# Kernel optimization log

Hardware: AMD Instinct MI355X
Metric: run time of the kernel (lower is better)

## Reference

```python
import jax, jax.numpy as jnp
import numpy as np
from jax import lax

N, E, G = 20000, 640000, 16
NA, H, NG, L, NC = 21, 128, 50, 6, 97
CUTOFF = 10.0
LOG2 = 0.6931471805599453

def ssp(v):
    # ShiftedSoftplus: softplus(x) - log(2)
    return jax.nn.softplus(v) - LOG2

def setup_inputs() -> dict:
    key = jax.random.key(0)
    ks = jax.random.split(key, 24)
    s = 0.08  # xavier-ish scale for 128-wide layers
    inp = {
        "x": jax.random.normal(ks[0], (N, NA), dtype=jnp.float32),
        "pos": jax.random.uniform(ks[1], (N, 3), dtype=jnp.float32, minval=0.0, maxval=30.0),
        "edge_index": jax.random.randint(ks[2], (2, E), 0, N, dtype=jnp.int64),
        "batch": jnp.sort(jax.random.randint(ks[3], (N,), 0, G, dtype=jnp.int64)),
        # embedding Linear(21 -> 128), weights stored [in, out]
        "emb_w": jax.random.normal(ks[4], (NA, H), dtype=jnp.float32) * 0.15,
        "emb_b": jnp.zeros((H,), dtype=jnp.float32),
        # per-interaction-block params, stacked over L layers
        "mlp1_w": jax.random.normal(ks[5], (L, NG, H), dtype=jnp.float32) * 0.12,
        "mlp1_b": jnp.zeros((L, H), dtype=jnp.float32),
        "mlp2_w": jax.random.normal(ks[6], (L, H, H), dtype=jnp.float32) * s,
        "mlp2_b": jnp.zeros((L, H), dtype=jnp.float32),
        "conv1_w": jax.random.normal(ks[7], (L, H, H), dtype=jnp.float32) * s,  # no bias
        "conv2_w": jax.random.normal(ks[8], (L, H, H), dtype=jnp.float32) * s,
        "conv2_b": jnp.zeros((L, H), dtype=jnp.float32),
        "lin_w": jax.random.normal(ks[9], (L, H, H), dtype=jnp.float32) * s,
        "lin_b": jnp.zeros((L, H), dtype=jnp.float32),
        # head (note: original reuses self.lin1 twice, act is ReLU, dropout eval=identity)
        "lin1_w": jax.random.normal(ks[10], (H, H), dtype=jnp.float32) * s,
        "lin1_b": jnp.zeros((H,), dtype=jnp.float32),
        "lin2_w": jax.random.normal(ks[11], (H, NC), dtype=jnp.float32) * s,
        "lin2_b": jnp.zeros((NC,), dtype=jnp.float32),
    }
    return inp

def reference(x, pos, edge_index, batch, emb_w, emb_b, mlp1_w, mlp1_b, mlp2_w,
              mlp2_b, conv1_w, conv2_w, conv2_b, lin_w, lin_b, lin1_w, lin1_b,
              lin2_w, lin2_b):
    row, col = edge_index[0], edge_index[1]  # source j, target i
    d = pos[row] - pos[col]                  # [E,3]
    edge_weight = jnp.sqrt(jnp.sum(d * d, axis=-1))  # [E]
    # Gaussian smearing
    offset = jnp.linspace(0.0, CUTOFF, NG)
    coeff = -0.5 / (offset[1] - offset[0]) ** 2
    edge_attr = jnp.exp(coeff * (edge_weight[:, None] - offset[None, :]) ** 2)  # [E,NG]
    # cosine cutoff
    C = 0.5 * (jnp.cos(edge_weight * jnp.pi / CUTOFF) + 1.0)  # [E]

    h = x @ emb_w + emb_b  # [N,H]

    def block(h, p):
        m1w, m1b, m2w, m2b, c1w, c2w, c2b, lw, lb = p
        # edge MLP filter times cutoff envelope
        Wf = (ssp(edge_attr @ m1w + m1b) @ m2w + m2b) * C[:, None]  # [E,H]
        hx = h @ c1w                                 # lin1 (no bias)
        msg = hx[row] * Wf                           # gather + modulate
        agg = jax.ops.segment_sum(msg, col, num_segments=N)  # scatter-add
        y = ssp(agg @ c2w + c2b)
        y = y @ lw + lb
        return h + y, None

    h, _ = lax.scan(block, h, (mlp1_w, mlp1_b, mlp2_w, mlp2_b,
                               conv1_w, conv2_w, conv2_b, lin_w, lin_b))

    h = jax.nn.relu(h @ lin1_w + lin1_b)
    # global mean pool
    ones = jnp.ones((N,), dtype=h.dtype)
    counts = jnp.maximum(jax.ops.segment_sum(ones, batch, num_segments=G), 1.0)
    graph_emb = jax.ops.segment_sum(h, batch, num_segments=G) / counts[:, None]  # [G,H]
    h2 = jax.nn.relu(graph_emb @ lin1_w + lin1_b)  # lin1 reused; dropout=identity (eval)
    out = h2 @ lin2_w + lin2_b                     # [G,NC]
    return graph_emb, out
```

## Files before the change

kernel.cpp:

```cpp
#include <hip/hip_runtime.h>
#include <hip/hip_bf16.h>

#define HD 128
#define NGAUSS 50
#define NLAYER 6
#define NGRAPH 16
#define NCLS 97
#define NTAB2 8192
#define WMAX 12.0f

typedef __attribute__((ext_vector_type(8))) short bf16x8;
typedef __attribute__((ext_vector_type(4))) float f32x4;
typedef __attribute__((ext_vector_type(8))) ushort u16x8;
typedef __attribute__((ext_vector_type(4))) ushort u16x4;

__device__ __forceinline__ float ssp_f(float x) {
    float e = __expf(-fabsf(x));
    return fmaxf(x, 0.0f) + __logf(0.5f + 0.5f * e);
}
__device__ __forceinline__ ushort f2bf(float f) {
    uint u = __float_as_uint(f);
    return (ushort)((u + 0x7FFFu + ((u >> 16) & 1u)) >> 16);
}
__device__ __forceinline__ float bf2f(ushort s) {
    return __uint_as_float(((uint)s) << 16);
}

__global__ void hist_kernel(const int* __restrict__ col, int* __restrict__ deg, int E) {
    int e = blockIdx.x * blockDim.x + threadIdx.x;
    if (e < E) atomicAdd(&deg[col[e]], 1);
}

__global__ void scan1_kernel(const int* __restrict__ deg, int* __restrict__ rowp,
                             int* __restrict__ bsum, int N) {
    __shared__ int sm[256];
    const int t = threadIdx.x, i = blockIdx.x * 256 + t;
    int v = (i < N) ? deg[i] : 0;
    sm[t] = v;
    __syncthreads();
    for (int off = 1; off < 256; off <<= 1) {
        int x = sm[t];
        int a = (t >= off) ? sm[t - off] : 0;
        __syncthreads();
        sm[t] = x + a;
        __syncthreads();
    }
    if (i < N) rowp[i] = sm[t] - v;
    if (t == 255) bsum[blockIdx.x] = sm[255];
}
__global__ void scan2_kernel(const int* __restrict__ bsum, int* __restrict__ boff,
                             int NB, int* __restrict__ rowpN) {
    __shared__ int sm[256];
    const int t = threadIdx.x;
    int v = (t < NB) ? bsum[t] : 0;
    sm[t] = v;
    __syncthreads();
    for (int off = 1; off < 256; off <<= 1) {
        int x = sm[t];
        int a = (t >= off) ? sm[t - off] : 0;
        __syncthreads();
        sm[t] = x + a;
        __syncthreads();
    }
    if (t < NB) boff[t] = sm[t] - v;
    if (t == 255) *rowpN = sm[255];
}
__global__ void scan3_kernel(int* __restrict__ rowp, const int* __restrict__ boff,
                             int* __restrict__ cursor, int N) {
    int i = blockIdx.x * blockDim.x + threadIdx.x;
    if (i < N) {
        int r = rowp[i] + boff[i >> 8];
        rowp[i] = r;
        cursor[i] = r;
    }
}

__global__ void fill_kernel(const int* __restrict__ row, const int* __restrict__ col,
                            const float* __restrict__ pos, int* __restrict__ cursor,
                            uint2* __restrict__ meta, int E) {
    int e = blockIdx.x * blockDim.x + threadIdx.x;
    if (e >= E) return;
    int c = col[e], r = row[e];
    int slot = atomicAdd(&cursor[c], 1);
    float dx = pos[r*3+0] - pos[c*3+0];
    float dy = pos[r*3+1] - pos[c*3+1];
    float dz = pos[r*3+2] - pos[c*3+2];
    float w = sqrtf(dx*dx + dy*dy + dz*dz);
    float cenv = 0.5f * (cosf(w * 0.31415926535897931f) + 1.0f);
    const float invDW = (float)(NTAB2 - 1) / WMAX;
    int i = (int)(w * invDW + 0.5f);
    i = min(i, NTAB2 - 1);
    uint w0 = ((uint)r) | (((uint)i) << 16);
    meta[slot] = make_uint2(w0, __float_as_uint(cenv));
}

__global__ void prep_kernel(const float* __restrict__ m1w, const float* __restrict__ c1w,
                            const float* __restrict__ c2w, const float* __restrict__ lw,
                            const float* __restrict__ l1w, const float* __restrict__ m2w,
                            ushort* __restrict__ m1T, ushort* __restrict__ nodeThi,
                            ushort* __restrict__ nodeTlo, ushort* __restrict__ m2T) {
    int idx = blockIdx.x * blockDim.x + threadIdx.x;
    const int S1 = 6*128*64, S2 = 19*128*128, S3 = 6*128*128;
    if (idx < S1) {
        int l = idx / 8192, r = idx % 8192, c = r / 64, k = r % 64;
        float v = (k < NGAUSS) ? m1w[(size_t)l*NGAUSS*128 + k*128 + c] : 0.0f;
        m1T[(size_t)l*8192 + c*64 + k] = f2bf(v);
    } else if (idx < S1 + S2) {
        int j = idx - S1;
        int m = j / 16384, r = j % 16384, c = r / 128, k = r % 128;
        const float* src;
        if (m < 6)       src = c1w + (size_t)m*16384;
        else if (m < 12) src = c2w + (size_t)(m-6)*16384;
        else if (m < 18) src = lw  + (size_t)(m-12)*16384;
        else             src = l1w;
        float v = src[k*128 + c];
        ushort hi = f2bf(v);
        nodeThi[(size_t)m*16384 + c*128 + k] = hi;
        nodeTlo[(size_t)m*16384 + c*128 + k] = f2bf(v - bf2f(hi));
    } else if (idx < S1 + S2 + S3) {
        int j = idx - S1 - S2;
        int l = j / 16384, r = j % 16384, c = r / 128, k = r % 128;
        m2T[(size_t)l*16384 + c*128 + k] = f2bf(m2w[(size_t)l*16384 + k*128 + c]);
    }
}

__global__ void embed_kernel(const float* __restrict__ x,
                             const float* __restrict__ emb_w, const float* __restrict__ emb_b,
                             float* __restrict__ h, int N) {
    int idx = blockIdx.x * blockDim.x + threadIdx.x;
    if (idx >= N * HD) return;
    int n = idx >> 7, t = idx & 127;
    float acc = emb_b[t];
    #pragma unroll
    for (int a = 0; a < 21; ++a) acc += x[n*21 + a] * emb_w[a*HD + t];
    h[idx] = acc;
}

__global__ __launch_bounds__(256, 2) void buildtab_kernel(
        const ushort* __restrict__ m1T_all, const ushort* __restrict__ m2T_all,
        const float* __restrict__ m1b_all, const float* __restrict__ m2b_all,
        ushort* __restrict__ Tb6) {
    __shared__ ushort A1[128 * 64];
    __shared__ ushort B1[128 * 64];
    __shared__ ushort U [128 * 128];
    char* A1b = (char*)A1;
    char* B1b = (char*)B1;
    char* Ub  = (char*)U;
    const int tid  = threadIdx.x;
    const int lane = tid & 63;
    const int wave = tid >> 6;
    const int l15  = lane & 15;
    const int kgrp = (lane >> 4) * 8;
    const int rbase = wave * 32;
    const int NTILES = NTAB2 / 128;
    const int layer = blockIdx.x / NTILES;
    const int mt    = blockIdx.x % NTILES;
    const ushort* m1T = m1T_all + (size_t)layer * 8192;
    const ushort* m2T = m2T_all + (size_t)layer * 16384;
    const float*  m1b = m1b_all + layer * HD;
    const float*  m2b = m2b_all + layer * HD;

    #pragma unroll
    for (int p = 0; p < 4; ++p) {
        int rr = p * 32 + (tid >> 3);
        int k8 = (tid & 7) * 8;
        u16x8 v = *reinterpret_cast<const u16x8*>(&m1T[(size_t)rr * 64 + k8]);
        *reinterpret_cast<u16x8*>(&B1b[rr*128 + ((2*k8) ^ ((rr & 7) << 4))]) = v;
    }

    float b1c[8], b2c[8];
    #pragma unroll
    for (int cb = 0; cb < 8; ++cb) { b1c[cb] = m1b[cb*16 + l15]; b2c[cb] = m2b[cb*16 + l15]; }

    const float step = 10.0f / 49.0f;
    const float coeff = -0.5f / (step * step);
    const float DW = WMAX / (float)(NTAB2 - 1);

    #pragma unroll
    for (int p = 0; p < 4; ++p) {
        int rr = p * 32 + (tid >> 3);
        int k8 = (tid & 7) * 8;
        float w = (float)(mt*128 + rr) * DW;
        u16x8 v;
        #pragma unroll
        for (int j = 0; j < 8; ++j) {
            int k = k8 + j;
            float d = w - (float)k * step;
            float g = (k < NGAUSS) ? __expf(coeff * d * d) : 0.0f;
            v[j] = f2bf(g);
        }
        *reinterpret_cast<u16x8*>(&A1b[rr*128 + ((2*k8) ^ ((rr & 7) << 4))]) = v;
    }
    __syncthreads();

    f32x4 acc1[2][8];
    #pragma unroll
    for (int i = 0; i < 2; ++i)
        #pragma unroll
        for (int j = 0; j < 8; ++j) { acc1[i][j].x=0.f; acc1[i][j].y=0.f; acc1[i][j].z=0.f; acc1[i][j].w=0.f; }
    #pragma unroll
    for (int ks = 0; ks < 2; ++ks) {
        int k = ks*32 + kgrp;
        bf16x8 af[2];
        #pragma unroll
        for (int rt = 0; rt < 2; ++rt) {
            int r = rbase + rt*16 + l15;
            af[rt] = *reinterpret_cast<const bf16x8*>(&A1b[r*128 + ((2*k) ^ ((r & 7) << 4))]);
        }
        #pragma unroll
        for (int cb = 0; cb < 8; ++cb) {
            int c = cb*16 + l15;
            bf16x8 bv = *reinterpret_cast<const bf16x8*>(&B1b[c*128 + ((2*k) ^ ((c & 7) << 4))]);
            acc1[0][cb] = __builtin_amdgcn_mfma_f32_16x16x32_bf16(af[0], bv, acc1[0][cb], 0, 0, 0);
            acc1[1][cb] = __builtin_amdgcn_mfma_f32_16x16x32_bf16(af[1], bv, acc1[1][cb], 0, 0, 0);
        }
    }
    #pragma unroll
    for (int rt = 0; rt < 2; ++rt) {
        #pragma unroll
        for (int cb = 0; cb < 8; ++cb) {
            int c = cb*16 + l15;
            #pragma unroll
            for (int i = 0; i < 4; ++i) {
                int rrow = rbase + rt*16 + (lane >> 4)*4 + i;
                ushort us = f2bf(ssp_f(acc1[rt][cb][i] + b1c[cb]));
                *reinterpret_cast<ushort*>(&Ub[rrow*256 + ((2*c) ^ ((rrow & 7) << 4))]) = us;
            }
        }
    }
    __syncthreads();

    f32x4 acc2[2][8];
    #pragma unroll
    for (int i = 0; i < 2; ++i)
        #pragma unroll
        for (int j = 0; j < 8; ++j) { acc2[i][j].x=0.f; acc2[i][j].y=0.f; acc2[i][j].z=0.f; acc2[i][j].w=0.f; }
    #pragma unroll
    for (int kh = 0; kh < 2; ++kh) {
        if (kh) __syncthreads();
        #pragma unroll
        for (int p = 0; p < 4; ++p) {
            int rr = p * 32 + (tid >> 3);
            int kk = (tid & 7) * 8;
            u16x8 v = *reinterpret_cast<const u16x8*>(&m2T[(size_t)rr*128 + kh*64 + kk]);
            *reinterpret_cast<u16x8*>(&A1b[rr*128 + ((2*kk) ^ ((rr & 7) << 4))]) = v;
        }
        __syncthreads();
        #pragma unroll
        for (int ks2 = 0; ks2 < 2; ++ks2) {
            int ku = kh*64 + ks2*32 + kgrp;
            int kb = ks2*32 + kgrp;
            bf16x8 af[2];
            #pragma unroll
            for (int rt = 0; rt < 2; ++rt) {
                int r = rbase + rt*16 + l15;
                af[rt] = *reinterpret_cast<const bf16x8*>(&Ub[r*256 + ((2*ku) ^ ((r & 7) << 4))]);
            }
            #pragma unroll
            for (int cb = 0; cb < 8; ++cb) {
                int c = cb*16 + l15;
                bf16x8 bv = *reinterpret_cast<const bf16x8*>(&A1b[c*128 + ((2*kb) ^ ((c & 7) << 4))]);
                acc2[0][cb] = __builtin_amdgcn_mfma_f32_16x16x32_bf16(af[0], bv, acc2[0][cb], 0, 0, 0);
                acc2[1][cb] = __builtin_amdgcn_mfma_f32_16x16x32_bf16(af[1], bv, acc2[1][cb], 0, 0, 0);
            }
        }
    }

    #pragma unroll
    for (int rt = 0; rt < 2; ++rt) {
        #pragma unroll
        for (int cb = 0; cb < 8; ++cb) {
            int c = cb*16 + l15;
            #pragma unroll
            for (int i = 0; i < 4; ++i) {
                int rrow = rbase + rt*16 + (lane >> 4)*4 + i;
                Tb6[((size_t)layer*NTAB2 + mt*128 + rrow) * HD + c] = f2bf(acc2[rt][cb][i] + b2c[cb]);
            }
        }
    }
}

template<int EPI>
__global__ __launch_bounds__(256) void gemv64_kernel(
        const float* __restrict__ A, const ushort* __restrict__ BThi,
        const ushort* __restrict__ BTlo, const float* __restrict__ bias,
        float* __restrict__ fdst, ushort* __restrict__ bdst, int mtiles) {
    __shared__ ushort Bw[128 * 256];
    __shared__ ushort A_[64 * 128];
    char* Bwb = (char*)Bw;
    char* Ab  = (char*)A_;
    const int tid  = threadIdx.x;
    const int lane = tid & 63;
    const int wave = tid >> 6;
    const int l15  = lane & 15;
    const int kgrp = (lane >> 4) * 8;
    const int rbase = wave * 16;

    #pragma unroll
    for (int p = 0; p < 16; ++p) {
        int idx = p * 256 + tid;
        int c = idx >> 5;
        int k8 = (idx & 31) * 8;
        const ushort* src = (k8 < 128) ? BThi : BTlo;
        u16x8 v = *reinterpret_cast<const u16x8*>(&src[(size_t)c*128 + (k8 & 127)]);
        *reinterpret_cast<u16x8*>(&Bwb[c*512 + ((2*k8) ^ ((c & 7) << 4))]) = v;
    }
    float bt[8];
    if (EPI == 4) {
        #pragma unroll
        for (int cb = 0; cb < 8; ++cb) bt[cb] = bias[cb*16 + l15];
    }
    __syncthreads();

    for (int mt = blockIdx.x; mt < mtiles; mt += gridDim.x) {
        #pragma unroll
        for (int p = 0; p < 8; ++p) {
            int rr = p * 8 + (tid >> 5);
            int k4 = (tid & 31) * 4;
            f32x4 v = *reinterpret_cast<const f32x4*>(&A[(size_t)(mt*64 + rr)*HD + k4]);
            u16x4 b;
            b.x = f2bf(v.x); b.y = f2bf(v.y); b.z = f2bf(v.z); b.w = f2bf(v.w);
            *reinterpret_cast<u16x4*>(&Ab[rr*256 + ((2*k4) ^ ((rr & 7) << 4))]) = b;
        }
        __syncthreads();

        bf16x8 af[4];
        {
            int r = rbase + l15;
            #pragma unroll
            for (int q = 0; q < 4; ++q)
                af[q] = *reinterpret_cast<const bf16x8*>(&Ab[r*256 + ((2*(q*32 + kgrp)) ^ ((r & 7) << 4))]);
        }
        f32x4 acc[8];
        #pragma unroll
        for (int j = 0; j < 8; ++j) { acc[j].x=0.f; acc[j].y=0.f; acc[j].z=0.f; acc[j].w=0.f; }
        #pragma unroll
        for (int ks = 0; ks < 8; ++ks) {
            int kB = ks*32 + kgrp;
            #pragma unroll
            for (int cb = 0; cb < 8; ++cb) {
                int c = cb*16 + l15;
                bf16x8 bv = *reinterpret_cast<const bf16x8*>(&Bwb[c*512 + ((2*kB) ^ ((c & 7) << 4))]);
                acc[cb] = __builtin_amdgcn_mfma_f32_16x16x32_bf16(af[ks & 3], bv, acc[cb], 0, 0, 0);
            }
        }

        #pragma unroll
        for (int cb = 0; cb < 8; ++cb) {
            int c = cb*16 + l15;
            #pragma unroll
            for (int i = 0; i < 4; ++i) {
                int row = mt*64 + rbase + (lane >> 4)*4 + i;
                size_t off = (size_t)row * HD + c;
                if (EPI == 4) fdst[off] = fmaxf(acc[cb][i] + bt[cb], 0.0f);
                else          bdst[off] = f2bf(acc[cb][i]);
            }
        }
        __syncthreads();
    }
}

__global__ __launch_bounds__(512, 1) void nodefused_kernel(
        const ushort* __restrict__ aggb,
        const ushort* __restrict__ c2hi, const ushort* __restrict__ c2lo,
        const float* __restrict__ c2b,
        const ushort* __restrict__ lwhi, const ushort* __restrict__ lwlo,
        const float* __restrict__ lb,
        float* __restrict__ h, int mtiles) {
    __shared__ ushort W1[128 * 256];
    __shared__ ushort W2[128 * 256];
    __shared__ ushort BUF[32 * 128];
    char* W1b = (char*)W1;
    char* W2b = (char*)W2;
    char* Bu  = (char*)BUF;
    const int tid  = threadIdx.x;
    const int lane = tid & 63;
    const int wave = tid >> 6;
    const int l15  = lane & 15;
    const int kgrp = (lane >> 4) * 8;
    const int wr = (wave & 1) * 16;
    const int wc = (wave >> 1) * 2;

    #pragma unroll
    for (int p = 0; p < 8; ++p) {
        int idx = p * 512 + tid;
        int c = idx >> 5;
        int k8 = (idx & 31) * 8;
        const ushort* s1 = (k8 < 128) ? c2hi : c2lo;
        u16x8 v1 = *reinterpret_cast<const u16x8*>(&s1[(size_t)c*128 + (k8 & 127)]);
        *reinterpret_cast<u16x8*>(&W1b[c*512 + ((2*k8) ^ ((c & 7) << 4))]) = v1;
        const ushort* s2 = (k8 < 128) ? lwhi : lwlo;
        u16x8 v2 = *reinterpret_cast<const u16x8*>(&s2[(size_t)c*128 + (k8 & 127)]);
        *reinterpret_cast<u16x8*>(&W2b[c*512 + ((2*k8) ^ ((c & 7) << 4))]) = v2;
    }
    float b1c[2], b2c[2];
    #pragma unroll
    for (int cb = 0; cb < 2; ++cb) {
        int c = (wc + cb)*16 + l15;
        b1c[cb] = c2b[c];
        b2c[cb] = lb[c];
    }
    __syncthreads();

    for (int mt = blockIdx.x; mt < mtiles; mt += gridDim.x) {
        {
            int rr = tid >> 4;
            int k8 = (tid & 15) * 8;
            u16x8 v = *reinterpret_cast<const u16x8*>(&aggb[(size_t)(mt*32 + rr)*HD + k8]);
            *reinterpret_cast<u16x8*>(&Bu[rr*256 + ((2*k8) ^ ((rr & 7) << 4))]) = v;
        }
        float hp[2][4];
        #pragma unroll
        for (int cb = 0; cb < 2; ++cb) {
            int c = (wc + cb)*16 + l15;
            #pragma unroll
            for (int i = 0; i < 4; ++i) {
                int row = mt*32 + wr + (lane >> 4)*4 + i;
                hp[cb][i] = h[(size_t)row * HD + c];
            }
        }
        __syncthreads();

        bf16x8 af[4];
        {
            int r = wr + l15;
            #pragma unroll
            for (int q = 0; q < 4; ++q)
                af[q] = *reinterpret_cast<const bf16x8*>(&Bu[r*256 + ((2*(q*32 + kgrp)) ^ ((r & 7) << 4))]);
        }
        f32x4 acc[2];
        #pragma unroll
        for (int j = 0; j < 2; ++j) { acc[j].x=0.f; acc[j].y=0.f; acc[j].z=0.f; acc[j].w=0.f; }
        #pragma unroll
        for (int ks = 0; ks < 8; ++ks) {
            int kB = ks*32 + kgrp;
            #pragma unroll
            for (int cb = 0; cb < 2; ++cb) {
                int c = (wc + cb)*16 + l15;
                bf16x8 bv = *reinterpret_cast<const bf16x8*>(&W1b[c*512 + ((2*kB) ^ ((c & 7) << 4))]);
                acc[cb] = __builtin_amdgcn_mfma_f32_16x16x32_bf16(af[ks & 3], bv, acc[cb], 0, 0, 0);
            }
        }
        __syncthreads();

        #pragma unroll
        for (int cb = 0; cb < 2; ++cb) {
            int c = (wc + cb)*16 + l15;
            #pragma unroll
            for (int i = 0; i < 4; ++i) {
                int rrow = wr + (lane >> 4)*4 + i;
                ushort us = f2bf(ssp_f(acc[cb][i] + b1c[cb]));
                *reinterpret_cast<ushort*>(&Bu[rrow*256 + ((2*c) ^ ((rrow & 7) << 4))]) = us;
            }
        }
        __syncthreads();

        {
            int r = wr + l15;
            #pragma unroll
            for (int q = 0; q < 4; ++q)
                af[q] = *reinterpret_cast<const bf16x8*>(&Bu[r*256 + ((2*(q*32 + kgrp)) ^ ((r & 7) << 4))]);
        }
        #pragma unroll
        for (int j = 0; j < 2; ++j) { acc[j].x=0.f; acc[j].y=0.f; acc[j].z=0.f; acc[j].w=0.f; }
        #pragma unroll
        for (int ks = 0; ks < 8; ++ks) {
            int kB = ks*32 + kgrp;
            #pragma unroll
            for (int cb = 0; cb < 2; ++cb) {
                int c = (wc + cb)*16 + l15;
                bf16x8 bv = *reinterpret_cast<const bf16x8*>(&W2b[c*512 + ((2*kB) ^ ((c & 7) << 4))]);
                acc[cb] = __builtin_amdgcn_mfma_f32_16x16x32_bf16(af[ks & 3], bv, acc[cb], 0, 0, 0);
            }
        }
        #pragma unroll
        for (int cb = 0; cb < 2; ++cb) {
            int c = (wc + cb)*16 + l15;
            #pragma unroll
            for (int i = 0; i < 4; ++i) {
                int row = mt*32 + wr + (lane >> 4)*4 + i;
                h[(size_t)row * HD + c] = hp[cb][i] + acc[cb][i] + b2c[cb];
            }
        }
        __syncthreads();
    }
}

__global__ __launch_bounds__(256) void gathersum_kernel(
        const ushort* __restrict__ Tb, const uint2* __restrict__ meta,
        const int* __restrict__ rowp, const ushort* __restrict__ hxb,
        ushort* __restrict__ aggb, int N) {
    const int lane = threadIdx.x & 63;
    const int n = blockIdx.x * 4 + (threadIdx.x >> 6);
    if (n >= N) return;
    const int c0 = lane * 2;
    const int s0 = rowp[n], s1 = rowp[n + 1];
    float al[4] = {0.f, 0.f, 0.f, 0.f};
    float ah[4] = {0.f, 0.f, 0.f, 0.f};
    int s = s0;
    for (; s + 8 <= s1; s += 8) {
        uint2 m[8];
        uint tv[8], hv[8];
        #pragma unroll
        for (int k = 0; k < 8; ++k) m[k] = meta[s + k];
        #pragma unroll
        for (int k = 0; k < 8; ++k) {
            tv[k] = *reinterpret_cast<const uint*>(&Tb[(size_t)(m[k].x >> 16) * HD + c0]);
            hv[k] = *reinterpret_cast<const uint*>(&hxb[(size_t)(m[k].x & 0xFFFFu) * HD + c0]);
        }
        #pragma unroll
        for (int k = 0; k < 8; ++k) {
            float cv = __uint_as_float(m[k].y);
            float glo = __uint_as_float(tv[k] << 16) * cv;
            float ghi = __uint_as_float(tv[k] & 0xFFFF0000u) * cv;
            al[k & 3] += glo * __uint_as_float(hv[k] << 16);
            ah[k & 3] += ghi * __uint_as_float(hv[k] & 0xFFFF0000u);
        }
    }
    for (; s < s1; ++s) {
        uint2 m0 = meta[s];
        uint tv = *reinterpret_cast<const uint*>(&Tb[(size_t)(m0.x >> 16) * HD + c0]);
        uint hv = *reinterpret_cast<const uint*>(&hxb[(size_t)(m0.x & 0xFFFFu) * HD + c0]);
        float cv = __uint_as_float(m0.y);
        al[0] += __uint_as_float(tv << 16) * cv * __uint_as_float(hv << 16);
        ah[0] += __uint_as_float(tv & 0xFFFF0000u) * cv * __uint_as_float(hv & 0xFFFF0000u);
    }
    float lo = (al[0] + al[1]) + (al[2] + al[3]);
    float hi = (ah[0] + ah[1]) + (ah[2] + ah[3]);
    uint out = ((uint)f2bf(lo)) | (((uint)f2bf(hi)) << 16);
    *reinterpret_cast<uint*>(&aggb[(size_t)n * HD + c0]) = out;
}

__global__ void pool_kernel(const float* __restrict__ h1, const int* __restrict__ batch,
                            float* __restrict__ gsum, float* __restrict__ gcnt, int N) {
    __shared__ float pool[NGRAPH][HD];
    __shared__ float cnt[NGRAPH];
    const int t = threadIdx.x;
    #pragma unroll
    for (int g = 0; g < NGRAPH; ++g) pool[g][t] = 0.0f;
    if (t < NGRAPH) cnt[t] = 0.0f;
    __syncthreads();
    int chunk = (N + gridDim.x - 1) / gridDim.x;
    int n0 = blockIdx.x * chunk, n1 = min(N, n0 + chunk);
    for (int n = n0; n < n1; ++n) {
        int b = batch[n];
        pool[b][t] += h1[(size_t)n * HD + t];
        if (t == 0) cnt[b] += 1.0f;
    }
    __syncthreads();
    #pragma unroll
    for (int g = 0; g < NGRAPH; ++g) atomicAdd(&gsum[g*HD + t], pool[g][t]);
    if (t < NGRAPH) atomicAdd(&gcnt[t], cnt[t]);
}

__global__ void finalize_kernel(const float* __restrict__ gsum, const float* __restrict__ gcnt,
                                const float* __restrict__ l1w, const float* __restrict__ l1b,
                                const float* __restrict__ l2w, const float* __restrict__ l2b,
                                float* __restrict__ d_out) {
    __shared__ float ge[HD];
    __shared__ float h2[HD];
    const int g = blockIdx.x, t = threadIdx.x;
    float cnt = fmaxf(gcnt[g], 1.0f);
    float v = gsum[g*HD + t] / cnt;
    d_out[g*HD + t] = v;
    ge[t] = v;
    __syncthreads();
    float acc = l1b[t];
    #pragma unroll 8
    for (int k = 0; k < HD; ++k) acc += ge[k] * l1w[k*HD + t];
    h2[t] = fmaxf(acc, 0.0f);
    __syncthreads();
    if (t < NCLS) {
        float o = l2b[t];
        #pragma unroll 8
        for (int k = 0; k < HD; ++k) o += h2[k] * l2w[k*NCLS + t];
        d_out[NGRAPH*HD + g*NCLS + t] = o;
    }
}

extern "C" void kernel_launch(void* const* d_in, const int* in_sizes, int n_in,
                              void* d_out, int out_size, void* d_ws, size_t ws_size,
                              hipStream_t stream) {
    const float* x     = (const float*)d_in[0];
    const float* pos   = (const float*)d_in[1];
    const int*   eidx  = (const int*)d_in[2];
    const int*   batch = (const int*)d_in[3];
    const float* emb_w = (const float*)d_in[4];
    const float* emb_b = (const float*)d_in[5];
    const float* m1w   = (const float*)d_in[6];
    const float* m1b   = (const float*)d_in[7];
    const float* m2w   = (const float*)d_in[8];
    const float* m2b   = (const float*)d_in[9];
    const float* c1w   = (const float*)d_in[10];
    const float* c2w   = (const float*)d_in[11];
    const float* c2b   = (const float*)d_in[12];
    const float* lw    = (const float*)d_in[13];
    const float* lb    = (const float*)d_in[14];
    const float* l1w   = (const float*)d_in[15];
    const float* l1b   = (const float*)d_in[16];
    const float* l2w   = (const float*)d_in[17];
    const float* l2b   = (const float*)d_in[18];

    const int N = in_sizes[0] / 21;
    const int E = in_sizes[2] / 2;
    const int* row = eidx;
    const int* col = eidx + E;
    const int NT64 = (N + 63) / 64;
    const int NT32 = (N + 31) / 32;
    const int NB   = (N + 255) / 256;
    const int Npad = NT64 * 64 + 64;

    size_t off = 0;
    char* base = (char*)d_ws;
    auto alloc = [&](size_t bytes) -> void* {
        off = (off + 255) & ~(size_t)255;
        void* p = base + off;
        off += bytes;
        return p;
    };
    int*    deg     = (int*)alloc((size_t)N * 4);
    int*    cursor  = (int*)alloc((size_t)N * 4);
    int*    rowp    = (int*)alloc((size_t)(N + 1) * 4);
    int*    bsum    = (int*)alloc(512 * 4);
    int*    boff    = (int*)alloc(512 * 4);
    uint2*  meta    = (uint2*)alloc((size_t)E * 8);
    float*  h       = (float*)alloc((size_t)Npad * HD * 4);
    ushort* hxb     = (ushort*)alloc((size_t)Npad * HD * 2);
    ushort* aggb    = (ushort*)alloc((size_t)Npad * HD * 2);
    float*  h1      = (float*)alloc((size_t)Npad * HD * 4);
    ushort* Tb6     = (ushort*)alloc((size_t)6 * NTAB2 * HD * 2);
    ushort* m1T     = (ushort*)alloc((size_t)6 * 128 * 64 * 2);
    ushort* nodeThi = (ushort*)alloc((size_t)19 * 128 * 128 * 2);
    ushort* nodeTlo = (ushort*)alloc((size_t)19 * 128 * 128 * 2);
    ushort* m2T     = (ushort*)alloc((size_t)6 * 128 * 128 * 2);
    float*  gsum    = (float*)alloc((size_t)NGRAPH * HD * 4);
    float*  gcnt    = (float*)alloc((size_t)NGRAPH * 4);

    prep_kernel<<<1792, 256, 0, stream>>>(m1w, c1w, c2w, lw, l1w, m2w,
                                          m1T, nodeThi, nodeTlo, m2T);
    hipMemsetAsync(deg, 0, (size_t)N * 4, stream);
    hist_kernel<<<(E + 255)/256, 256, 0, stream>>>(col, deg, E);
    scan1_kernel<<<NB, 256, 0, stream>>>(deg, rowp, bsum, N);
    scan2_kernel<<<1, 256, 0, stream>>>(bsum, boff, NB, rowp + N);
    scan3_kernel<<<NB, 256, 0, stream>>>(rowp, boff, cursor, N);
    fill_kernel<<<(E + 255)/256, 256, 0, stream>>>(row, col, pos, cursor, meta, E);
    buildtab_kernel<<<6 * (NTAB2/128), 256, 0, stream>>>(m1T, m2T, m1b, m2b, Tb6);
    embed_kernel<<<(N*HD + 255)/256, 256, 0, stream>>>(x, emb_w, emb_b, h, N);

    gemv64_kernel<5><<<NT64, 256, 0, stream>>>(h, nodeThi, nodeTlo, nullptr,
                                               nullptr, hxb, NT64);

    for (int l = 0; l < NLAYER; ++l) {
        const ushort* c2Thi = nodeThi + (size_t)(6 + l) * 16384;
        const ushort* c2Tlo = nodeTlo + (size_t)(6 + l) * 16384;
        const ushort* lThi  = nodeThi + (size_t)(12 + l) * 16384;
        const ushort* lTlo  = nodeTlo + (size_t)(12 + l) * 16384;

        gathersum_kernel<<<(N + 3)/4, 256, 0, stream>>>(
            Tb6 + (size_t)l * NTAB2 * HD, meta, rowp, hxb, aggb, N);

        nodefused_kernel<<<256, 512, 0, stream>>>(
            aggb, c2Thi, c2Tlo, c2b + l*HD, lThi, lTlo, lb + l*HD, h, NT32);

        if (l < NLAYER - 1) {
            gemv64_kernel<5><<<NT64, 256, 0, stream>>>(
                h, nodeThi + (size_t)(l + 1) * 16384, nodeTlo + (size_t)(l + 1) * 16384,
                nullptr, nullptr, hxb, NT64);
        } else {
            gemv64_kernel<4><<<NT64, 256, 0, stream>>>(
                h, nodeThi + (size_t)18 * 16384, nodeTlo + (size_t)18 * 16384,
                l1b, h1, nullptr, NT64);
        }
    }

    hipMemsetAsync(gsum, 0, (size_t)(NGRAPH*HD + NGRAPH) * 4, stream);
    pool_kernel<<<256, HD, 0, stream>>>(h1, batch, gsum, gcnt, N);
    finalize_kernel<<<NGRAPH, HD, 0, stream>>>(gsum, gcnt, l1w, l1b, l2w, l2b,
                                               (float*)d_out);
}
```

Measured before the change: 455.2 us.

## Fold cosine cutoff envelope into filter table and shrink edge metadata

Multiplies the cosine cutoff envelope into the precomputed per-distance filter table, using the quantized table distance in place of the exact edge distance. Each edge's metadata then shrinks from 8 bytes to 4 and the per-edge multiply in the gather loop goes away. The gather loop is also unrolled to 16 edges, with a 4-edge middle tail. The envelope now depends on the quantized distance, which adds a small approximation error, and the wider unroll raises register use.

```diff
diff --git a/kernel.cpp b/kernel.cpp
--- a/kernel.cpp
+++ b/kernel.cpp
@@ -77,7 +77,7 @@
 
 __global__ void fill_kernel(const int* __restrict__ row, const int* __restrict__ col,
                             const float* __restrict__ pos, int* __restrict__ cursor,
-                            uint2* __restrict__ meta, int E) {
+                            uint* __restrict__ meta, int E) {
     int e = blockIdx.x * blockDim.x + threadIdx.x;
     if (e >= E) return;
     int c = col[e], r = row[e];
@@ -86,12 +86,10 @@
     float dy = pos[r*3+1] - pos[c*3+1];
     float dz = pos[r*3+2] - pos[c*3+2];
     float w = sqrtf(dx*dx + dy*dy + dz*dz);
-    float cenv = 0.5f * (cosf(w * 0.31415926535897931f) + 1.0f);
     const float invDW = (float)(NTAB2 - 1) / WMAX;
     int i = (int)(w * invDW + 0.5f);
     i = min(i, NTAB2 - 1);
-    uint w0 = ((uint)r) | (((uint)i) << 16);
-    meta[slot] = make_uint2(w0, __float_as_uint(cenv));
+    meta[slot] = ((uint)r) | (((uint)i) << 16);
 }
 
 __global__ void prep_kernel(const float* __restrict__ m1w, const float* __restrict__ c1w,
@@ -274,7 +272,10 @@
             #pragma unroll
             for (int i = 0; i < 4; ++i) {
                 int rrow = rbase + rt*16 + (lane >> 4)*4 + i;
-                Tb6[((size_t)layer*NTAB2 + mt*128 + rrow) * HD + c] = f2bf(acc2[rt][cb][i] + b2c[cb]);
+                float w = (float)(mt*128 + rrow) * DW;
+                float cv = 0.5f * (cosf(w * 0.31415926535897931f) + 1.0f);
+                Tb6[((size_t)layer*NTAB2 + mt*128 + rrow) * HD + c] =
+                    f2bf((acc2[rt][cb][i] + b2c[cb]) * cv);
             }
         }
     }
@@ -487,7 +488,7 @@
 }
 
 __global__ __launch_bounds__(256) void gathersum_kernel(
-        const ushort* __restrict__ Tb, const uint2* __restrict__ meta,
+        const ushort* __restrict__ Tb, const uint* __restrict__ meta,
         const int* __restrict__ rowp, const ushort* __restrict__ hxb,
         ushort* __restrict__ aggb, int N) {
     const int lane = threadIdx.x & 63;
@@ -498,32 +499,42 @@
     float al[4] = {0.f, 0.f, 0.f, 0.f};
     float ah[4] = {0.f, 0.f, 0.f, 0.f};
     int s = s0;
-    for (; s + 8 <= s1; s += 8) {
-        uint2 m[8];
-        uint tv[8], hv[8];
-        #pragma unroll
-        for (int k = 0; k < 8; ++k) m[k] = meta[s + k];
-        #pragma unroll
-        for (int k = 0; k < 8; ++k) {
-            tv[k] = *reinterpret_cast<const uint*>(&Tb[(size_t)(m[k].x >> 16) * HD + c0]);
-            hv[k] = *reinterpret_cast<const uint*>(&hxb[(size_t)(m[k].x & 0xFFFFu) * HD + c0]);
-        }
-        #pragma unroll
-        for (int k = 0; k < 8; ++k) {
-            float cv = __uint_as_float(m[k].y);
-            float glo = __uint_as_float(tv[k] << 16) * cv;
-            float ghi = __uint_as_float(tv[k] & 0xFFFF0000u) * cv;
-            al[k & 3] += glo * __uint_as_float(hv[k] << 16);
-            ah[k & 3] += ghi * __uint_as_float(hv[k] & 0xFFFF0000u);
+    for (; s + 16 <= s1; s += 16) {
+        uint m[16], tv[16], hv[16];
+        #pragma unroll
+        for (int k = 0; k < 16; ++k) m[k] = meta[s + k];
+        #pragma unroll
+        for (int k = 0; k < 16; ++k) {
+            tv[k] = *reinterpret_cast<const uint*>(&Tb[(size_t)(m[k] >> 16) * HD + c0]);
+            hv[k] = *reinterpret_cast<const uint*>(&hxb[(size_t)(m[k] & 0xFFFFu) * HD + c0]);
+        }
+        #pragma unroll
+        for (int k = 0; k < 16; ++k) {
+            al[k & 3] += __uint_as_float(tv[k] << 16) * __uint_as_float(hv[k] << 16);
+            ah[k & 3] += __uint_as_float(tv[k] & 0xFFFF0000u) * __uint_as_float(hv[k] & 0xFFFF0000u);
+        }
+    }
+    for (; s + 4 <= s1; s += 4) {
+        uint m[4], tv[4], hv[4];
+        #pragma unroll
+        for (int k = 0; k < 4; ++k) m[k] = meta[s + k];
+        #pragma unroll
+        for (int k = 0; k < 4; ++k) {
+            tv[k] = *reinterpret_cast<const uint*>(&Tb[(size_t)(m[k] >> 16) * HD + c0]);
+            hv[k] = *reinterpret_cast<const uint*>(&hxb[(size_t)(m[k] & 0xFFFFu) * HD + c0]);
+        }
+        #pragma unroll
+        for (int k = 0; k < 4; ++k) {
+            al[k] += __uint_as_float(tv[k] << 16) * __uint_as_float(hv[k] << 16);
+            ah[k] += __uint_as_float(tv[k] & 0xFFFF0000u) * __uint_as_float(hv[k] & 0xFFFF0000u);
         }
     }
     for (; s < s1; ++s) {
-        uint2 m0 = meta[s];
-        uint tv = *reinterpret_cast<const uint*>(&Tb[(size_t)(m0.x >> 16) * HD + c0]);
-        uint hv = *reinterpret_cast<const uint*>(&hxb[(size_t)(m0.x & 0xFFFFu) * HD + c0]);
-        float cv = __uint_as_float(m0.y);
-        al[0] += __uint_as_float(tv << 16) * cv * __uint_as_float(hv << 16);
-        ah[0] += __uint_as_float(tv & 0xFFFF0000u) * cv * __uint_as_float(hv & 0xFFFF0000u);
+        uint m0 = meta[s];
+        uint tv = *reinterpret_cast<const uint*>(&Tb[(size_t)(m0 >> 16) * HD + c0]);
+        uint hv = *reinterpret_cast<const uint*>(&hxb[(size_t)(m0 & 0xFFFFu) * HD + c0]);
+        al[0] += __uint_as_float(tv << 16) * __uint_as_float(hv << 16);
+        ah[0] += __uint_as_float(tv & 0xFFFF0000u) * __uint_as_float(hv & 0xFFFF0000u);
     }
     float lo = (al[0] + al[1]) + (al[2] + al[3]);
     float hi = (ah[0] + ah[1]) + (ah[2] + ah[3]);
@@ -623,7 +634,7 @@
     int*    rowp    = (int*)alloc((size_t)(N + 1) * 4);
     int*    bsum    = (int*)alloc(512 * 4);
     int*    boff    = (int*)alloc(512 * 4);
-    uint2*  meta    = (uint2*)alloc((size_t)E * 8);
+    uint*   meta    = (uint*)alloc((size_t)E * 4);
     float*  h       = (float*)alloc((size_t)Npad * HD * 4);
     ushort* hxb     = (ushort*)alloc((size_t)Npad * HD * 2);
     ushort* aggb    = (ushort*)alloc((size_t)Npad * HD * 2);
```

Result: no change. 460.5 us (+1.1%).
